# Kernel optimization log

Measured on AMD Instinct MI355X. Metric: run time of the kernel, lower is better.

## Reference

```python
import jax, jax.numpy as jnp
import numpy as np

EMB = 2048
HEADS = 16


def setup_inputs() -> dict:
    key = jax.random.key(0)
    k_x, k_wqkv, k_bqkv, k_wo, k_bo = jax.random.split(key, 5)
    B, S, E = 2, 2048, EMB
    x = jax.random.normal(k_x, (B, S, E), dtype=jnp.float32)
    # nn.Linear weights stored as (in, out) for x @ W + b convention
    W_qkv = jax.random.normal(k_wqkv, (E, 3 * E), dtype=jnp.float32) * 0.02
    b_qkv = jax.random.normal(k_bqkv, (3 * E,), dtype=jnp.float32) * 0.02
    W_out = jax.random.normal(k_wo, (E, E), dtype=jnp.float32) * 0.02
    b_out = jax.random.normal(k_bo, (E,), dtype=jnp.float32) * 0.02
    return {"x": x, "W_qkv": W_qkv, "b_qkv": b_qkv, "W_out": W_out, "b_out": b_out}


def reference(x, W_qkv, b_qkv, W_out, b_out):
    B, S, E = x.shape
    H = HEADS
    dh = E // H
    # QKV projection: (B,S,3E)
    qkv = x @ W_qkv + b_qkv
    # Faithful to torch: reshape (B,S,H,3*dh) THEN split -> interleaved per-head q/k/v
    qkv = qkv.reshape(B, S, H, 3 * dh).transpose(0, 2, 1, 3)  # (B,H,S,3*dh)
    q, k, v = jnp.split(qkv, 3, axis=-1)  # each (B,H,S,dh)
    q = q / jnp.asarray(dh, q.dtype) ** 0.5
    scores = jnp.einsum('bhqd,bhkd->bhqk', q, k)  # (B,H,S,S)
    weights = jax.nn.softmax(scores, axis=-1)
    attn = jnp.einsum('bhqk,bhkd->bhqd', weights, v)  # (B,H,S,dh)
    attn = attn.transpose(0, 2, 1, 3).reshape(B, S, E)
    return attn @ W_out + b_out
```

## Files before the change

### kernel.cpp

```cpp
#include <hip/hip_runtime.h>
#include <type_traits>
#include <utility>

#define DI __device__ __forceinline__

typedef unsigned short u16;
typedef float f32x4 __attribute__((ext_vector_type(4)));
typedef float f32x16 __attribute__((ext_vector_type(16)));
typedef short s16x8 __attribute__((ext_vector_type(8)));
typedef __bf16 bf16x8 __attribute__((ext_vector_type(8)));

template <typename V, typename = void>
struct mfma_ok : std::false_type {};
template <typename V>
struct mfma_ok<V, std::void_t<decltype(__builtin_amdgcn_mfma_f32_16x16x32_bf16(
    std::declval<V>(), std::declval<V>(), std::declval<f32x4>(), 0, 0, 0))>>
    : std::true_type {};
using frag_t = std::conditional_t<mfma_ok<bf16x8>::value, bf16x8, s16x8>;

union U128 {
  int4 i;
  frag_t f;
  u16 s[8];
};

DI f32x4 mfma16(const U128& a, const U128& b, f32x4 c) {
  return __builtin_amdgcn_mfma_f32_16x16x32_bf16(a.f, b.f, c, 0, 0, 0);
}
DI f32x16 mfma32(const U128& a, const U128& b, f32x16 c) {
  return __builtin_amdgcn_mfma_f32_32x32x16_bf16(a.f, b.f, c, 0, 0, 0);
}

DI u16 f2b(float x) {
  union { float f; unsigned u; } v; v.f = x;
  unsigned r = v.u + 0x7FFFu + ((v.u >> 16) & 1u);
  return (u16)(r >> 16);
}

DI unsigned pk2bf(float a, float b) {
  unsigned short ua = __builtin_bit_cast(unsigned short, (__bf16)a);
  unsigned short ub = __builtin_bit_cast(unsigned short, (__bf16)b);
  return (unsigned)ua | ((unsigned)ub << 16);
}

#if __has_builtin(__builtin_amdgcn_exp2f)
#define EXP2F __builtin_amdgcn_exp2f
#else
#define EXP2F exp2f
#endif

DI void plswap(unsigned& lo, unsigned& hi) {
  asm("v_permlane32_swap_b32 %0, %1" : "+v"(lo), "+v"(hi));
}

typedef __attribute__((address_space(1))) void gas_t;
typedef __attribute__((address_space(3))) void las_t;
DI void gll16(const void* g, void* l) {
  __builtin_amdgcn_global_load_lds((gas_t*)g, (las_t*)l, 16, 0, 0);
}

#define QSCALE 0.12751791437603762f

__global__ __launch_bounds__(256) void k_conv_bf16(const float* __restrict__ in,
                                                   u16* __restrict__ out, int n4) {
  int i = blockIdx.x * 256 + threadIdx.x;
  if (i >= n4) return;
  float4 v = ((const float4*)in)[i];
  ushort4 o;
  o.x = f2b(v.x); o.y = f2b(v.y); o.z = f2b(v.z); o.w = f2b(v.w);
  ((ushort4*)out)[i] = o;
}

__global__ __launch_bounds__(256) void k_transpose_f2b(const float* __restrict__ in,
                                                       u16* __restrict__ out,
                                                       int R, int C) {
  __shared__ __attribute__((aligned(16))) u16 Tb[64][68];
  int t = threadIdx.x;
  long r0 = (long)blockIdx.y * 64, c0 = (long)blockIdx.x * 64;
  int cq = (t & 15) * 4, rr = t >> 4;
#pragma unroll
  for (int it = 0; it < 4; ++it) {
    int r = rr + it * 16;
    float4 v = *(const float4*)(in + (r0 + r) * C + c0 + cq);
    Tb[r][cq + 0] = f2b(v.x); Tb[r][cq + 1] = f2b(v.y);
    Tb[r][cq + 2] = f2b(v.z); Tb[r][cq + 3] = f2b(v.w);
  }
  __syncthreads();
#pragma unroll
  for (int it = 0; it < 2; ++it) {
    int ci = it * 256 + t;
    int cc = ci >> 3, ch = ci & 7, rb = ch * 8;
    unsigned p0 = Tb[rb + 0][cc] | ((unsigned)Tb[rb + 1][cc] << 16);
    unsigned p1 = Tb[rb + 2][cc] | ((unsigned)Tb[rb + 3][cc] << 16);
    unsigned p2 = Tb[rb + 4][cc] | ((unsigned)Tb[rb + 5][cc] << 16);
    unsigned p3 = Tb[rb + 6][cc] | ((unsigned)Tb[rb + 7][cc] << 16);
    *(int4*)(out + (c0 + cc) * R + r0 + rb) = make_int4(p0, p1, p2, p3);
  }
}

template <int MODE>
__global__ __launch_bounds__(256, 4) void k_gemm_bt(const u16* __restrict__ A,
                                                    const u16* __restrict__ Bt,
                                                    const float* __restrict__ bias,
                                                    void* __restrict__ Cout,
                                                    u16* __restrict__ qb,
                                                    u16* __restrict__ kbv,
                                                    u16* __restrict__ vb,
                                                    int M, int N, int K) {
  __shared__ __attribute__((aligned(16))) u16 As[128 * 64];
  __shared__ __attribute__((aligned(16))) u16 Bs[128 * 64];
  int t = threadIdx.x;
  int lane = t & 63, w = t >> 6, quad = lane >> 4, l15 = lane & 15;
  long m0 = (long)blockIdx.y * 128, n0 = (long)blockIdx.x * 128;
  int wr = (w >> 1) * 64, wc = (w & 1) * 64;
  int sw = l15 & 7;
  f32x4 acc[4][4] = {};
  for (int k0 = 0; k0 < K; k0 += 64) {
    __syncthreads();
#pragma unroll
    for (int it = 0; it < 4; ++it) {
      int ci = it * 256 + t;
      int row = ci >> 3, cl = (ci & 7) ^ (row & 7);
      gll16(A + (m0 + row) * K + k0 + cl * 8, As + ci * 8);
      gll16(Bt + (n0 + row) * K + k0 + cl * 8, Bs + ci * 8);
    }
    __syncthreads();
#pragma unroll
    for (int kk = 0; kk < 2; ++kk) {
      U128 a[4], b[4];
#pragma unroll
      for (int i = 0; i < 4; ++i)
        a[i].i = *(const int4*)(As + (wr + i * 16 + l15) * 64 + (((kk * 4 + quad) ^ sw) << 3));
#pragma unroll
      for (int j = 0; j < 4; ++j)
        b[j].i = *(const int4*)(Bs + (wc + j * 16 + l15) * 64 + (((kk * 4 + quad) ^ sw) << 3));
#pragma unroll
      for (int i = 0; i < 4; ++i)
#pragma unroll
        for (int j = 0; j < 4; ++j)
          acc[i][j] = mfma16(a[i], b[j], acc[i][j]);
    }
  }
  float bj[4];
#pragma unroll
  for (int j = 0; j < 4; ++j) bj[j] = bias[n0 + wc + j * 16 + l15];

  int hidx = (int)(n0 / 384);
  int rsel = (int)(n0 - hidx * 384) >> 7;
  u16* route = (MODE == 1) ? (rsel == 0 ? qb : rsel == 1 ? kbv : vb) : nullptr;

#pragma unroll
  for (int i = 0; i < 4; ++i) {
#pragma unroll
    for (int rr2 = 0; rr2 < 4; ++rr2) {
      long row = m0 + wr + i * 16 + quad * 4 + rr2;
#pragma unroll
      for (int j = 0; j < 4; ++j) {
        float v = acc[i][j][rr2] + bj[j];
        if (MODE == 1) {
          if (rsel == 0) v *= QSCALE;
          int bidx = (int)(row >> 11), s = (int)(row & 2047);
          long obase = ((long)(bidx * 16 + hidx) * 2048 + s) * 128;
          int dh = wc + j * 16 + l15;
          unsigned pb = f2b(v);
          unsigned other = __shfl_xor(pb, 1);
          if (!(l15 & 1))
            ((unsigned*)route)[(obase + dh) >> 1] = pb | (other << 16);
        } else {
          long col = n0 + wc + j * 16 + l15;
          unsigned bits = __float_as_uint(v);
          unsigned other = __shfl_xor(bits, 1);
          if (!(l15 & 1)) {
            uint2 pr; pr.x = bits; pr.y = other;
            *(uint2*)((float*)Cout + row * N + col) = pr;
          }
        }
      }
    }
  }
}

__global__ __launch_bounds__(256) void k_extract_vt(const u16* __restrict__ vb,
                                                    u16* __restrict__ vt) {
  __shared__ __attribute__((aligned(16))) u16 Vb[64][136];
  int t = threadIdx.x;
  int s0 = blockIdx.x * 64;
  int bh = blockIdx.y;
  long inbase = ((long)bh * 2048 + s0) * 128;
#pragma unroll
  for (int it = 0; it < 4; ++it) {
    int ci = it * 256 + t;
    int s = ci >> 4, ch = ci & 15;
    int4 v = *(const int4*)(vb + inbase + s * 128 + ch * 8);
    *(int4*)(&Vb[s][ch * 8]) = v;
  }
  __syncthreads();
  long outbase = (long)bh * 128 * 2048 + s0;
#pragma unroll
  for (int it = 0; it < 4; ++it) {
    int ci = it * 256 + t;
    int d = ci >> 3, ch = ci & 7, sb = ch * 8;
    unsigned p0 = Vb[sb + 0][d] | ((unsigned)Vb[sb + 1][d] << 16);
    unsigned p1 = Vb[sb + 2][d] | ((unsigned)Vb[sb + 3][d] << 16);
    unsigned p2 = Vb[sb + 4][d] | ((unsigned)Vb[sb + 5][d] << 16);
    unsigned p3 = Vb[sb + 6][d] | ((unsigned)Vb[sb + 7][d] << 16);
    *(int4*)(vt + outbase + (long)d * 2048 + sb) = make_int4(p0, p1, p2, p3);
  }
}

__global__ __launch_bounds__(256, 2) void k_flash(const u16* __restrict__ qb,
                                                  const u16* __restrict__ kb,
                                                  const u16* __restrict__ vt,
                                                  u16* __restrict__ attn) {
  __shared__ __attribute__((aligned(16))) u16 Ks[2][64 * 128];
  __shared__ __attribute__((aligned(16))) u16 Vts[2][128 * 64];
  int t = threadIdx.x;
  int lane = t & 63, w = t >> 6, l31 = lane & 31, h = lane >> 5;
  int q0 = blockIdx.x * 128 + w * 32;
  int bh = blockIdx.y, b = bh >> 4, hd = bh & 15;

  const u16* qbase = qb + ((long)bh * 2048 + q0 + l31) * 128;
  U128 qf[8];
#pragma unroll
  for (int dht = 0; dht < 8; ++dht)
    qf[dht].i = *(const int4*)(qbase + dht * 16 + h * 8);
  __syncthreads();

  f32x16 O[4] = {};
  float lsum = 0.f;
  const u16* kbh = kb + (long)bh * 2048 * 128;
  long vbase = (long)bh * 128 * 2048;

  auto stage = [&](int buf, int k0) {
#pragma unroll
    for (int it = 0; it < 4; ++it) {
      int ci = it * 256 + t;
      int key = ci >> 4, cp = ci & 15, cl = cp ^ (key & 7);
      gll16(kbh + (long)(k0 + key) * 128 + cl * 8, &Ks[buf][0] + ci * 8);
    }
#pragma unroll
    for (int it = 0; it < 4; ++it) {
      int ci = it * 256 + t;
      int d = ci >> 3, cp = ci & 7, cl = cp ^ (d & 7);
      gll16(vt + vbase + (long)d * 2048 + k0 + cl * 8, &Vts[buf][0] + ci * 8);
    }
  };

  stage(0, 0);
  int cur = 0;
  for (int k0 = 0; k0 < 2048; k0 += 64) {
    if (k0 + 64 < 2048) {
      stage(cur ^ 1, k0 + 64);
      asm volatile("s_waitcnt vmcnt(8)" ::: "memory");
    } else {
      asm volatile("s_waitcnt vmcnt(0)" ::: "memory");
    }
    __builtin_amdgcn_s_barrier();
    asm volatile("" ::: "memory");
    const u16* Kb = &Ks[cur][0];
    const u16* Vb = &Vts[cur][0];

    f32x16 St[2] = {};
    __builtin_amdgcn_s_setprio(1);
#pragma unroll
    for (int kb2 = 0; kb2 < 2; ++kb2) {
      int row = kb2 * 32 + l31, sw = row & 7;
      const u16* kr = Kb + row * 128;
#pragma unroll
      for (int dht = 0; dht < 8; ++dht) {
        U128 kf;
        kf.i = *(const int4*)(kr + (((dht * 2 + h) ^ sw) << 3));
        St[kb2] = mfma32(kf, qf[dht], St[kb2]);
      }
    }
    __builtin_amdgcn_s_setprio(0);

    float pk[2][16];
#pragma unroll
    for (int kb2 = 0; kb2 < 2; ++kb2)
#pragma unroll
      for (int r = 0; r < 16; ++r) {
        float p = EXP2F(St[kb2][r]);
        pk[kb2][r] = p;
        lsum += p;
      }

    U128 pf[4];
#pragma unroll
    for (int kb2 = 0; kb2 < 2; ++kb2)
#pragma unroll
      for (int g = 0; g < 2; ++g) {
        const float* p = &pk[kb2][g * 8];
        unsigned w0 = pk2bf(p[0], p[1]);
        unsigned w1 = pk2bf(p[2], p[3]);
        unsigned w2 = pk2bf(p[4], p[5]);
        unsigned w3 = pk2bf(p[6], p[7]);
        plswap(w0, w2);
        plswap(w1, w3);
        pf[kb2 * 2 + g].i = make_int4(w0, w1, w2, w3);
      }

    __builtin_amdgcn_s_setprio(1);
#pragma unroll
    for (int kt = 0; kt < 4; ++kt)
#pragma unroll
      for (int dht = 0; dht < 4; ++dht) {
        int vrow = dht * 32 + l31, vsw = vrow & 7;
        U128 vf;
        vf.i = *(const int4*)(Vb + vrow * 64 + (((kt * 2 + h) ^ vsw) << 3));
        O[dht] = mfma32(vf, pf[kt], O[dht]);
      }
    __builtin_amdgcn_s_setprio(0);

    asm volatile("" ::: "memory");
    __builtin_amdgcn_s_barrier();
    cur ^= 1;
  }

  float ltot = lsum + __shfl_xor(lsum, 32);
  float inv = 1.f / ltot;
  long orow = (long)b * 2048 + q0 + l31;
  u16* ob = attn + orow * 2048 + hd * 128;
#pragma unroll
  for (int dht = 0; dht < 4; ++dht)
#pragma unroll
    for (int g = 0; g < 4; ++g) {
      int dh = dht * 32 + g * 8 + h * 4;
      float v0 = O[dht][4 * g + 0] * inv, v1 = O[dht][4 * g + 1] * inv;
      float v2 = O[dht][4 * g + 2] * inv, v3 = O[dht][4 * g + 3] * inv;
      uint2 pkd;
      pkd.x = pk2bf(v0, v1);
      pkd.y = pk2bf(v2, v3);
      *(uint2*)(ob + dh) = pkd;
    }
}

extern "C" void kernel_launch(void* const* d_in, const int* in_sizes, int n_in,
                              void* d_out, int out_size, void* d_ws, size_t ws_size,
                              hipStream_t stream) {
  const float* x    = (const float*)d_in[0];
  const float* Wqkv = (const float*)d_in[1];
  const float* bqkv = (const float*)d_in[2];
  const float* Wout = (const float*)d_in[3];
  const float* bout = (const float*)d_in[4];
  float* out = (float*)d_out;
  char* ws = (char*)d_ws;

  if (ws_size < 75497472u) return;

  u16* xb    = (u16*)d_out;
  u16* wqkvt = (u16*)(ws);
  u16* qbuf  = (u16*)(ws + 25165824);
  u16* kbuf  = (u16*)(ws + 41943040);
  u16* vbuf  = (u16*)(ws + 58720256);
  u16* vtb   = (u16*)d_out;
  u16* woutt = (u16*)(ws);
  u16* attnb = (u16*)(ws + 8388608);

  k_conv_bf16<<<8192, 256, 0, stream>>>(x, xb, 2097152);
  k_transpose_f2b<<<dim3(96, 32), 256, 0, stream>>>(Wqkv, wqkvt, 2048, 6144);
  k_gemm_bt<1><<<dim3(48, 32), 256, 0, stream>>>(xb, wqkvt, bqkv, nullptr,
                                                 qbuf, kbuf, vbuf, 4096, 6144, 2048);
  k_extract_vt<<<dim3(32, 32), 256, 0, stream>>>(vbuf, vtb);
  k_transpose_f2b<<<dim3(32, 32), 256, 0, stream>>>(Wout, woutt, 2048, 2048);
  k_flash<<<dim3(16, 32), 256, 0, stream>>>(qbuf, kbuf, vtb, attnb);
  k_gemm_bt<0><<<dim3(16, 32), 256, 0, stream>>>(attnb, woutt, bout, out,
                                                 nullptr, nullptr, nullptr, 4096, 2048, 2048);
}
```

Baseline: 388.0 us.

## Add double-buffered 256x256-tile GEMM for most of the QKV projection

Adds a 512-thread GEMM kernel with 256x256 output tiles and double-buffered LDS staging, so the next K-slice loads while MFMAs run on the current one. It covers the first 4096 columns of the QKV projection. The remaining 2048 columns still use the original 128-tile kernel, which gains a column-offset argument. The goal is more data reuse per block and overlap of global loads with compute. The cost is very large LDS use (one block per CU) and two launches for one GEMM.

```diff
diff --git a/kernel.cpp b/kernel.cpp
--- a/kernel.cpp
+++ b/kernel.cpp
@@ -99,6 +99,110 @@
 }
 
 template <int MODE>
+__global__ __launch_bounds__(512, 2) void k_gemm8p(const u16* __restrict__ A,
+                                                   const u16* __restrict__ Bt,
+                                                   const float* __restrict__ bias,
+                                                   void* __restrict__ Cout,
+                                                   u16* __restrict__ qb,
+                                                   u16* __restrict__ kbv,
+                                                   u16* __restrict__ vb,
+                                                   int M, int N, int K) {
+  __shared__ __attribute__((aligned(16))) u16 As[2][256 * 64];
+  __shared__ __attribute__((aligned(16))) u16 Bs[2][256 * 64];
+  int t = threadIdx.x;
+  int lane = t & 63, w = t >> 6, quad = lane >> 4, l15 = lane & 15;
+  long m0 = (long)blockIdx.y * 256, n0 = (long)blockIdx.x * 256;
+  int wr = (w >> 2) * 128;
+  int wc = (w & 3) * 64;
+  int sw = l15 & 7;
+  f32x4 acc[8][4] = {};
+
+  auto stage = [&](int buf, int k0) {
+#pragma unroll
+    for (int it = 0; it < 4; ++it) {
+      int ci = it * 512 + t;
+      int row = ci >> 3, cl = (ci & 7) ^ (row & 7);
+      gll16(A + (m0 + row) * K + k0 + cl * 8, &As[buf][0] + ci * 8);
+    }
+#pragma unroll
+    for (int it = 0; it < 4; ++it) {
+      int ci = it * 512 + t;
+      int row = ci >> 3, cl = (ci & 7) ^ (row & 7);
+      gll16(Bt + (n0 + row) * K + k0 + cl * 8, &Bs[buf][0] + ci * 8);
+    }
+  };
+
+  stage(0, 0);
+  int nk = K >> 6;
+  for (int i = 0; i < nk; ++i) {
+    int c = i & 1;
+    asm volatile("s_waitcnt vmcnt(0) lgkmcnt(0)" ::: "memory");
+    __builtin_amdgcn_s_barrier();
+    asm volatile("" ::: "memory");
+    if (i + 1 < nk) stage(c ^ 1, (i + 1) << 6);
+    const u16* Ab = &As[c][0];
+    const u16* Bb = &Bs[c][0];
+#pragma unroll
+    for (int kk = 0; kk < 2; ++kk) {
+      U128 a[8], b[4];
+#pragma unroll
+      for (int i2 = 0; i2 < 8; ++i2)
+        a[i2].i = *(const int4*)(Ab + (wr + i2 * 16 + l15) * 64 + (((kk * 4 + quad) ^ sw) << 3));
+#pragma unroll
+      for (int j = 0; j < 4; ++j)
+        b[j].i = *(const int4*)(Bb + (wc + j * 16 + l15) * 64 + (((kk * 4 + quad) ^ sw) << 3));
+      __builtin_amdgcn_s_setprio(1);
+#pragma unroll
+      for (int i2 = 0; i2 < 8; ++i2)
+#pragma unroll
+        for (int j = 0; j < 4; ++j)
+          acc[i2][j] = mfma16(a[i2], b[j], acc[i2][j]);
+      __builtin_amdgcn_s_setprio(0);
+    }
+    asm volatile("" ::: "memory");
+  }
+
+  float bj[4];
+#pragma unroll
+  for (int j = 0; j < 4; ++j) bj[j] = bias[n0 + wc + j * 16 + l15];
+
+  int grp = (int)(n0 >> 7) + (wc >> 7);
+  int hidx = grp / 3, rsel = grp - hidx * 3;
+  u16* route = (MODE == 1) ? (rsel == 0 ? qb : rsel == 1 ? kbv : vb) : nullptr;
+  int dbase = (int)((n0 + wc) & 127);
+
+#pragma unroll
+  for (int i = 0; i < 8; ++i) {
+#pragma unroll
+    for (int rr2 = 0; rr2 < 4; ++rr2) {
+      long row = m0 + wr + i * 16 + quad * 4 + rr2;
+#pragma unroll
+      for (int j = 0; j < 4; ++j) {
+        float v = acc[i][j][rr2] + bj[j];
+        if (MODE == 1) {
+          if (rsel == 0) v *= QSCALE;
+          int bidx = (int)(row >> 11), s = (int)(row & 2047);
+          long obase = ((long)(bidx * 16 + hidx) * 2048 + s) * 128;
+          int dh = dbase + j * 16 + l15;
+          unsigned pb = f2b(v);
+          unsigned other = __shfl_xor(pb, 1);
+          if (!(l15 & 1))
+            ((unsigned*)route)[(obase + dh) >> 1] = pb | (other << 16);
+        } else {
+          long col = n0 + wc + j * 16 + l15;
+          unsigned bits = __float_as_uint(v);
+          unsigned other = __shfl_xor(bits, 1);
+          if (!(l15 & 1)) {
+            uint2 pr; pr.x = bits; pr.y = other;
+            *(uint2*)((float*)Cout + row * (long)N + col) = pr;
+          }
+        }
+      }
+    }
+  }
+}
+
+template <int MODE>
 __global__ __launch_bounds__(256, 4) void k_gemm_bt(const u16* __restrict__ A,
                                                     const u16* __restrict__ Bt,
                                                     const float* __restrict__ bias,
@@ -106,12 +210,13 @@
                                                     u16* __restrict__ qb,
                                                     u16* __restrict__ kbv,
                                                     u16* __restrict__ vb,
+                                                    int n_off,
                                                     int M, int N, int K) {
   __shared__ __attribute__((aligned(16))) u16 As[128 * 64];
   __shared__ __attribute__((aligned(16))) u16 Bs[128 * 64];
   int t = threadIdx.x;
   int lane = t & 63, w = t >> 6, quad = lane >> 4, l15 = lane & 15;
-  long m0 = (long)blockIdx.y * 128, n0 = (long)blockIdx.x * 128;
+  long m0 = (long)blockIdx.y * 128, n0 = n_off + (long)blockIdx.x * 128;
   int wr = (w >> 1) * 64, wc = (w & 1) * 64;
   int sw = l15 & 7;
   f32x4 acc[4][4] = {};
@@ -359,11 +464,13 @@
 
   k_conv_bf16<<<8192, 256, 0, stream>>>(x, xb, 2097152);
   k_transpose_f2b<<<dim3(96, 32), 256, 0, stream>>>(Wqkv, wqkvt, 2048, 6144);
-  k_gemm_bt<1><<<dim3(48, 32), 256, 0, stream>>>(xb, wqkvt, bqkv, nullptr,
-                                                 qbuf, kbuf, vbuf, 4096, 6144, 2048);
+  k_gemm8p<1><<<dim3(16, 16), 512, 0, stream>>>(xb, wqkvt, bqkv, nullptr,
+                                                qbuf, kbuf, vbuf, 4096, 6144, 2048);
+  k_gemm_bt<1><<<dim3(16, 32), 256, 0, stream>>>(xb, wqkvt, bqkv, nullptr,
+                                                 qbuf, kbuf, vbuf, 4096, 4096, 6144, 2048);
   k_extract_vt<<<dim3(32, 32), 256, 0, stream>>>(vbuf, vtb);
   k_transpose_f2b<<<dim3(32, 32), 256, 0, stream>>>(Wout, woutt, 2048, 2048);
   k_flash<<<dim3(16, 32), 256, 0, stream>>>(qbuf, kbuf, vtb, attnb);
   k_gemm_bt<0><<<dim3(16, 32), 256, 0, stream>>>(attnb, woutt, bout, out,
-                                                 nullptr, nullptr, nullptr, 4096, 2048, 2048);
-}
+                                                 nullptr, nullptr, nullptr, 0, 4096, 2048, 2048);
+}
```

Measured after the change: 377.1 us. 2.8% less time.
